# Kernel optimization log

Measured on AMD Instinct MI355X. Metric: run time of the kernel, lower is better.

The kernel has to match this reference:

```python
import jax, jax.numpy as jnp
import numpy as np

H, DK, DV, D = 16, 64, 64, 1024  # num_heads, dk, dv, model_dim (H*DV == D)
B, S = 4, 2048

def setup_inputs() -> dict:
    key = jax.random.key(0)
    ks = jax.random.split(key, 10)
    sc = 0.02
    x  = jax.random.normal(ks[0], (B, S, D), dtype=jnp.float32)
    Wq = jax.random.normal(ks[1], (H, D, DK), dtype=jnp.float32) * sc
    bq = jax.random.normal(ks[2], (H, DK), dtype=jnp.float32) * sc
    Wk = jax.random.normal(ks[3], (H, D, DK), dtype=jnp.float32) * sc
    bk = jax.random.normal(ks[4], (H, DK), dtype=jnp.float32) * sc
    Wv = jax.random.normal(ks[5], (H, D, DV), dtype=jnp.float32) * sc
    bv = jax.random.normal(ks[6], (H, DV), dtype=jnp.float32) * sc
    Wo = jax.random.normal(ks[7], (H * DV, D), dtype=jnp.float32) * sc
    bo = jax.random.normal(ks[8], (D,), dtype=jnp.float32) * sc
    return {"x": x, "Wq": Wq, "bq": bq, "Wk": Wk, "bk": bk,
            "Wv": Wv, "bv": bv, "Wo": Wo, "bo": bo}

def reference(x, Wq, bq, Wk, bk, Wv, bv, Wo, bo):
    # Batched per-head projections: [B,S,D] x [H,D,dk] -> [B,H,S,dk]
    Qx = jnp.einsum('bsd,hdk->bhsk', x, Wq) + bq[None, :, None, :]
    Kx = jnp.einsum('bsd,hdk->bhsk', x, Wk) + bk[None, :, None, :]
    Vx = jnp.einsum('bsd,hdv->bhsv', x, Wv) + bv[None, :, None, :]
    scores = jnp.einsum('bhsk,bhtk->bhst', Qx, Kx) / jnp.sqrt(jnp.float32(DK))
    attn = jax.nn.softmax(scores, axis=-1)
    out = jnp.einsum('bhst,bhtv->bhsv', attn, Vx)  # [B,H,S,dv]
    # concat heads (head order matches the torch cat order) -> [B,S,H*dv]
    cat = out.transpose(0, 2, 1, 3).reshape(B, S, H * DV)
    return cat @ Wo + bo
```

## Files before the change

kernel.cpp:

```cpp
#include <hip/hip_runtime.h>
#include <hip/hip_bf16.h>
#include <stdint.h>

typedef __bf16 bf16;
typedef __bf16 bf16x8 __attribute__((ext_vector_type(8)));
typedef __bf16 bf16x4 __attribute__((ext_vector_type(4)));
typedef float  f32x4  __attribute__((ext_vector_type(4)));
typedef float  f32x16 __attribute__((ext_vector_type(16)));

#define H_   16
#define D_   1024
#define B_   4
#define S_   2048
#define M_   (B_*S_)
#define REGION 8388608LL

#define QSCALE 0.18033688011112042f


__global__ void cast_x_kernel(const float* __restrict__ x, bf16* __restrict__ xb) {
    const int i = blockIdx.x * 256 + threadIdx.x;
    const float4* src = reinterpret_cast<const float4*>(x) + (size_t)i * 2;
    float4 a = src[0], b = src[1];
    bf16x8 o;
    o[0]=(bf16)a.x; o[1]=(bf16)a.y; o[2]=(bf16)a.z; o[3]=(bf16)a.w;
    o[4]=(bf16)b.x; o[5]=(bf16)b.y; o[6]=(bf16)b.z; o[7]=(bf16)b.w;
    *reinterpret_cast<bf16x8*>(xb + (size_t)i * 8) = o;
}

__global__ void prep_wqkv_kernel(const float* __restrict__ Wq, const float* __restrict__ Wk,
                                 const float* __restrict__ Wv, const float* __restrict__ bq,
                                 const float* __restrict__ bk, const float* __restrict__ bv,
                                 bf16* __restrict__ WqkvT, float* __restrict__ qkvb) {
    const int t = blockIdx.x * 256 + threadIdx.x;
    const int n = t >> 7, d0 = (t & 127) << 3;
    const int which = n >> 10, hh = (n >> 6) & 15, dk = n & 63;
    const float* W = (which == 0) ? Wq : (which == 1) ? Wk : Wv;
    const float* src = W + (size_t)hh * 65536 + (size_t)d0 * 64 + dk;
    bf16x8 o;
#pragma unroll
    for (int i = 0; i < 8; ++i) o[i] = (bf16)src[(size_t)i * 64];
    *reinterpret_cast<bf16x8*>(WqkvT + (size_t)n * D_ + d0) = o;
    if (d0 == 0) {
        const float* bb = (which == 0) ? bq : (which == 1) ? bk : bv;
        qkvb[n] = bb[n & 1023];
    }
}

__global__ void prep_wo_kernel(const float* __restrict__ Wo, bf16* __restrict__ WoT) {
    __shared__ float tile[64][65];
    const int k0 = blockIdx.x * 64, n0 = blockIdx.y * 64;
    const int t = threadIdx.x;
#pragma unroll
    for (int i = 0; i < 16; ++i) {
        int idx = t + i * 256, r = idx >> 6, c = idx & 63;
        tile[r][c] = Wo[(size_t)(k0 + r) * D_ + n0 + c];
    }
    __syncthreads();
#pragma unroll
    for (int i = 0; i < 16; ++i) {
        int idx = t + i * 256, n = idx >> 6, k = idx & 63;
        WoT[(size_t)(n0 + n) * D_ + k0 + k] = (bf16)tile[k][n];
    }
}

template <int MODE>
__global__ __launch_bounds__(256, 2)
void gemm_kernel(const bf16* __restrict__ A, const bf16* __restrict__ Bt,
                 const float* __restrict__ bias, void* __restrict__ Cout) {
    const int K = 1024;
    __shared__ __attribute__((aligned(16))) uint8_t ldsb[32768];
    const int t = threadIdx.x, w = t >> 6, ln = t & 63;
    const int g = ln >> 4, c = ln & 15;
    const int wm = w >> 1, wn = w & 1;
    const int bm = blockIdx.x, bn = blockIdx.y;

    const bf16* Ab = A  + (size_t)bm * 128 * K;
    const bf16* Bb = Bt + (size_t)bn * 128 * K;

    f32x4 zero = {0.f, 0.f, 0.f, 0.f};
    f32x4 acc[4][4];
#pragma unroll
    for (int mi = 0; mi < 4; ++mi)
#pragma unroll
        for (int ni = 0; ni < 4; ++ni) acc[mi][ni] = zero;

    const int srow = ln >> 3;
    const int scol = ((ln & 7) ^ srow) * 8;

    for (int kt = 0; kt < 16; ++kt) {
        const int k0 = kt * 64;
        __syncthreads();
#pragma unroll
        for (int i = 0; i < 4; ++i) {
            const int call = w * 4 + i;
            const int row = call * 8 + srow;
            const bf16* ga = Ab + (size_t)row * K + k0 + scol;
            const bf16* gb = Bb + (size_t)row * K + k0 + scol;
            __builtin_amdgcn_global_load_lds(
                (const __attribute__((address_space(1))) void*)ga,
                (__attribute__((address_space(3))) void*)(ldsb + call * 1024), 16, 0, 0);
            __builtin_amdgcn_global_load_lds(
                (const __attribute__((address_space(1))) void*)gb,
                (__attribute__((address_space(3))) void*)(ldsb + 16384 + call * 1024), 16, 0, 0);
        }
        __syncthreads();
#pragma unroll
        for (int kc = 0; kc < 2; ++kc) {
            bf16x8 af[4], bfr[4];
#pragma unroll
            for (int mi = 0; mi < 4; ++mi) {
                const int lrow = wm * 64 + mi * 16 + c;
                const int cb = (kc * 64 + g * 16) ^ ((lrow & 7) << 4);
                af[mi] = *reinterpret_cast<const bf16x8*>(ldsb + lrow * 128 + cb);
            }
#pragma unroll
            for (int ni = 0; ni < 4; ++ni) {
                const int lrow = wn * 64 + ni * 16 + c;
                const int cb = (kc * 64 + g * 16) ^ ((lrow & 7) << 4);
                bfr[ni] = *reinterpret_cast<const bf16x8*>(ldsb + 16384 + lrow * 128 + cb);
            }
#pragma unroll
            for (int mi = 0; mi < 4; ++mi)
#pragma unroll
                for (int ni = 0; ni < 4; ++ni)
                    acc[mi][ni] = __builtin_amdgcn_mfma_f32_16x16x32_bf16(
                        af[mi], bfr[ni], acc[mi][ni], 0, 0, 0);
        }
    }

#pragma unroll
    for (int mi = 0; mi < 4; ++mi) {
#pragma unroll
        for (int ni = 0; ni < 4; ++ni) {
            const int mrow = bm * 128 + wm * 64 + mi * 16 + g * 4;
            const int ncol = bn * 128 + wn * 64 + ni * 16 + c;
            const float bv_ = bias[ncol];
            if (MODE == 0) {
                const int which = ncol >> 10, hh = (ncol >> 6) & 15, dk = ncol & 63;
                const size_t bh64 = (size_t)((mrow >> 11) * 16 + hh);
                const int sI = mrow & 2047;
                if (which == 2) {
                    bf16x4 p4;
#pragma unroll
                    for (int j = 0; j < 4; ++j) p4[j] = (bf16)(acc[mi][ni][j] + bv_);
                    *reinterpret_cast<bf16x4*>((bf16*)Cout + 2 * REGION +
                                               (bh64 * 64 + dk) * S_ + sI) = p4;
                } else {
                    const float sc = (which == 0) ? QSCALE : 1.0f;
                    bf16* dst = (bf16*)Cout + (size_t)which * REGION +
                                (bh64 * S_ + sI) * 64 + dk;
#pragma unroll
                    for (int j = 0; j < 4; ++j)
                        dst[(size_t)j * 64] = (bf16)((acc[mi][ni][j] + bv_) * sc);
                }
            } else {
#pragma unroll
                for (int j = 0; j < 4; ++j)
                    ((float*)Cout)[(size_t)(mrow + j) * D_ + ncol] = acc[mi][ni][j] + bv_;
            }
        }
    }
}


__global__ __launch_bounds__(256, 4)
void attn_kernel(const bf16* __restrict__ Q, const bf16* __restrict__ K,
                 const bf16* __restrict__ Vt, bf16* __restrict__ cat) {
    __shared__ __attribute__((aligned(16))) bf16 KsA[2][64 * 64];
    __shared__ __attribute__((aligned(16))) bf16 VsA[2][64 * 64];
    __shared__ float red[4][32];
    const int t = threadIdx.x, w = t >> 6, lane = t & 63;
    const int l31 = lane & 31, h = lane >> 5;

    const int bid = blockIdx.x;
    const int nid = (bid & 7) * 128 + (bid >> 3);
    const int bh = nid >> 4, qb = nid & 15;
    const int q0 = qb * 128 + w * 32;

    const bf16* Qg = Q  + ((size_t)bh * S_ + q0) * 64;
    const bf16* Kg = K  + (size_t)bh * S_ * 64;
    const bf16* Vg = Vt + (size_t)bh * 64 * S_;

    bf16x8 qf[4];
#pragma unroll
    for (int dc = 0; dc < 4; ++dc)
        qf[dc] = *reinterpret_cast<const bf16x8*>(Qg + (size_t)l31 * 64 + dc * 16 + h * 8);

    const int sr = lane >> 3, ss = lane & 7;
    const int swz = (ss ^ sr) * 8;

    auto STAGE_KV = [&](int buf, int kv0) {
#pragma unroll
        for (int cc = 0; cc < 2; ++cc) {
            const int row = w * 16 + cc * 8;
            const int rr = row + sr;
            const int rs = (rr & ~12) | ((rr & 4) << 1) | ((rr & 8) >> 1);
            __builtin_amdgcn_global_load_lds(
                (const __attribute__((address_space(1))) void*)
                    (Kg + (size_t)(kv0 + rs) * 64 + swz),
                (__attribute__((address_space(3))) void*)(&KsA[buf][row * 64]), 16, 0, 0);
            __builtin_amdgcn_global_load_lds(
                (const __attribute__((address_space(1))) void*)
                    (Vg + (size_t)(rr) * S_ + kv0 + swz),
                (__attribute__((address_space(3))) void*)(&VsA[buf][row * 64]), 16, 0, 0);
        }
    };

    f32x16 o0, o1;
#pragma unroll
    for (int j = 0; j < 16; ++j) { o0[j] = 0.f; o1[j] = 0.f; }
    float lsum = 0.f;

    STAGE_KV(0, 0);
    for (int it = 0; it < 32; ++it) {
        __syncthreads();
        if (it + 1 < 32) STAGE_KV((it + 1) & 1, (it + 1) * 64);
        const bf16* ks = KsA[it & 1];
        const bf16* vs = VsA[it & 1];
#pragma unroll
        for (int kb = 0; kb < 2; ++kb) {
            f32x16 s;
#pragma unroll
            for (int j = 0; j < 16; ++j) s[j] = 0.f;
#pragma unroll
            for (int dc = 0; dc < 4; ++dc) {
                const int row = kb * 32 + l31;
                const int slot = (2 * dc + h) ^ (row & 7);
                bf16x8 kf = *reinterpret_cast<const bf16x8*>(ks + row * 64 + slot * 8);
                s = __builtin_amdgcn_mfma_f32_32x32x16_bf16(kf, qf[dc], s, 0, 0, 0);
            }
            float pf[16];
#pragma unroll
            for (int j = 0; j < 16; ++j) {
                pf[j] = __builtin_amdgcn_exp2f(s[j]);
                lsum += pf[j];
            }
            bf16x8 af0, af1;
#pragma unroll
            for (int e = 0; e < 8; ++e) { af0[e] = (bf16)pf[e]; af1[e] = (bf16)pf[8 + e]; }
#pragma unroll
            for (int t2 = 0; t2 < 2; ++t2) {
#pragma unroll
                for (int nb = 0; nb < 2; ++nb) {
                    const int row = l31 + 32 * nb;
                    const int slot = (4 * kb + 2 * t2 + h) ^ (row & 7);
                    bf16x8 vf = *reinterpret_cast<const bf16x8*>(vs + row * 64 + slot * 8);
                    if (nb == 0)
                        o0 = __builtin_amdgcn_mfma_f32_32x32x16_bf16(
                            t2 ? af1 : af0, vf, o0, 0, 0, 0);
                    else
                        o1 = __builtin_amdgcn_mfma_f32_32x32x16_bf16(
                            t2 ? af1 : af0, vf, o1, 0, 0, 0);
                }
            }
        }
    }

    lsum += __shfl_xor(lsum, 32, 64);
    if (h == 0) red[w][l31] = 1.0f / lsum;
    const int b = bh >> 4, hh = bh & 15;
#pragma unroll
    for (int j = 0; j < 16; ++j) {
        const int q = (j & 3) + 8 * (j >> 2) + 4 * h;
        const float rr = red[w][q];
        bf16* dst = cat + ((size_t)b * S_ + q0 + q) * D_ + hh * 64 + l31;
        dst[0]  = (bf16)(o0[j] * rr);
        dst[32] = (bf16)(o1[j] * rr);
    }
}

extern "C" void kernel_launch(void* const* d_in, const int* in_sizes, int n_in,
                              void* d_out, int out_size, void* d_ws, size_t ws_size,
                              hipStream_t stream) {
    const float* x  = (const float*)d_in[0];
    const float* Wq = (const float*)d_in[1];
    const float* bq = (const float*)d_in[2];
    const float* Wk = (const float*)d_in[3];
    const float* bk = (const float*)d_in[4];
    const float* Wv = (const float*)d_in[5];
    const float* bv = (const float*)d_in[6];
    const float* Wo = (const float*)d_in[7];
    const float* bo = (const float*)d_in[8];
    float* out = (float*)d_out;
    char* ws = (char*)d_ws;

    bf16*  xb    = (bf16*)(ws);
    bf16*  cat   = (bf16*)(ws + 16777216LL);
    bf16*  WqkvT = (bf16*)(ws + 33554432LL);
    bf16*  WoT   = (bf16*)(ws + 39845888LL);
    float* qkvb  = (float*)(ws + 41943040LL);
    bf16*  Qb    = (bf16*)(ws + 41955328LL);
    bf16*  Kb    = Qb + REGION;
    bf16*  Vtb   = Qb + 2 * REGION;

    hipLaunchKernelGGL(cast_x_kernel, dim3(4096), dim3(256), 0, stream, x, xb);
    hipLaunchKernelGGL(prep_wqkv_kernel, dim3(1536), dim3(256), 0, stream,
                       Wq, Wk, Wv, bq, bk, bv, WqkvT, qkvb);
    hipLaunchKernelGGL(prep_wo_kernel, dim3(16, 16), dim3(256), 0, stream, Wo, WoT);
    hipLaunchKernelGGL((gemm_kernel<0>), dim3(64, 24), dim3(256), 0, stream,
                       xb, WqkvT, qkvb, (void*)Qb);
    hipLaunchKernelGGL(attn_kernel, dim3(1024), dim3(256), 0, stream, Qb, Kb, Vtb, cat);
    hipLaunchKernelGGL((gemm_kernel<1>), dim3(64, 8), dim3(256), 0, stream,
                       cat, WoT, bo, (void*)out);
}
```

Baseline: 191.2 us.

## Process two query tiles per wave in attention to reuse K/V fragments

Each wave in the attention kernel now handles 64 query rows as two 32-row MFMA tiles instead of one. K and V fragments read from LDS are shared across both tiles, roughly halving LDS traffic per unit of MFMA work. The grid halves to 512 blocks, launch bounds drop to 2 blocks per CU, and s_setprio hints are wrapped around the MFMA bursts. The cost is more accumulator registers per thread and fewer blocks to hide latency.

After: 192.2 us. About the same (+0.5%).

```diff
diff --git a/kernel.cpp b/kernel.cpp
--- a/kernel.cpp
+++ b/kernel.cpp
@@ -164,28 +164,31 @@
 }
 
 
-__global__ __launch_bounds__(256, 4)
+__global__ __launch_bounds__(256, 2)
 void attn_kernel(const bf16* __restrict__ Q, const bf16* __restrict__ K,
                  const bf16* __restrict__ Vt, bf16* __restrict__ cat) {
     __shared__ __attribute__((aligned(16))) bf16 KsA[2][64 * 64];
     __shared__ __attribute__((aligned(16))) bf16 VsA[2][64 * 64];
-    __shared__ float red[4][32];
+    __shared__ float red[4][64];
     const int t = threadIdx.x, w = t >> 6, lane = t & 63;
     const int l31 = lane & 31, h = lane >> 5;
 
     const int bid = blockIdx.x;
-    const int nid = (bid & 7) * 128 + (bid >> 3);
-    const int bh = nid >> 4, qb = nid & 15;
-    const int q0 = qb * 128 + w * 32;
+    const int nid = (bid & 7) * 64 + (bid >> 3);
+    const int bh = nid >> 3, qb = nid & 7;
+    const int q0 = qb * 256 + w * 64;
 
     const bf16* Qg = Q  + ((size_t)bh * S_ + q0) * 64;
     const bf16* Kg = K  + (size_t)bh * S_ * 64;
     const bf16* Vg = Vt + (size_t)bh * 64 * S_;
 
-    bf16x8 qf[4];
-#pragma unroll
-    for (int dc = 0; dc < 4; ++dc)
-        qf[dc] = *reinterpret_cast<const bf16x8*>(Qg + (size_t)l31 * 64 + dc * 16 + h * 8);
+    bf16x8 qf[2][4];
+#pragma unroll
+    for (int qt = 0; qt < 2; ++qt)
+#pragma unroll
+        for (int dc = 0; dc < 4; ++dc)
+            qf[qt][dc] = *reinterpret_cast<const bf16x8*>(
+                Qg + (size_t)(qt * 32 + l31) * 64 + dc * 16 + h * 8);
 
     const int sr = lane >> 3, ss = lane & 7;
     const int swz = (ss ^ sr) * 8;
@@ -207,10 +210,13 @@
         }
     };
 
-    f32x16 o0, o1;
-#pragma unroll
-    for (int j = 0; j < 16; ++j) { o0[j] = 0.f; o1[j] = 0.f; }
-    float lsum = 0.f;
+    f32x16 o[2][2];
+    f32x16 lsv[2];
+#pragma unroll
+    for (int qt = 0; qt < 2; ++qt) {
+#pragma unroll
+        for (int j = 0; j < 16; ++j) { o[qt][0][j] = 0.f; o[qt][1][j] = 0.f; lsv[qt][j] = 0.f; }
+    }
 
     STAGE_KV(0, 0);
     for (int it = 0; it < 32; ++it) {
@@ -220,25 +226,37 @@
         const bf16* vs = VsA[it & 1];
 #pragma unroll
         for (int kb = 0; kb < 2; ++kb) {
-            f32x16 s;
-#pragma unroll
-            for (int j = 0; j < 16; ++j) s[j] = 0.f;
+            bf16x8 kf[4];
 #pragma unroll
             for (int dc = 0; dc < 4; ++dc) {
                 const int row = kb * 32 + l31;
                 const int slot = (2 * dc + h) ^ (row & 7);
-                bf16x8 kf = *reinterpret_cast<const bf16x8*>(ks + row * 64 + slot * 8);
-                s = __builtin_amdgcn_mfma_f32_32x32x16_bf16(kf, qf[dc], s, 0, 0, 0);
-            }
-            float pf[16];
-#pragma unroll
-            for (int j = 0; j < 16; ++j) {
-                pf[j] = __builtin_amdgcn_exp2f(s[j]);
-                lsum += pf[j];
-            }
-            bf16x8 af0, af1;
-#pragma unroll
-            for (int e = 0; e < 8; ++e) { af0[e] = (bf16)pf[e]; af1[e] = (bf16)pf[8 + e]; }
+                kf[dc] = *reinterpret_cast<const bf16x8*>(ks + row * 64 + slot * 8);
+            }
+            f32x16 s0, s1;
+#pragma unroll
+            for (int j = 0; j < 16; ++j) { s0[j] = 0.f; s1[j] = 0.f; }
+            __builtin_amdgcn_s_setprio(1);
+#pragma unroll
+            for (int dc = 0; dc < 4; ++dc) {
+                s0 = __builtin_amdgcn_mfma_f32_32x32x16_bf16(kf[dc], qf[0][dc], s0, 0, 0, 0);
+                s1 = __builtin_amdgcn_mfma_f32_32x32x16_bf16(kf[dc], qf[1][dc], s1, 0, 0, 0);
+            }
+            __builtin_amdgcn_s_setprio(0);
+            f32x16 p0, p1;
+#pragma unroll
+            for (int j = 0; j < 16; ++j) p0[j] = __builtin_amdgcn_exp2f(s0[j]);
+#pragma unroll
+            for (int j = 0; j < 16; ++j) p1[j] = __builtin_amdgcn_exp2f(s1[j]);
+            lsv[0] += p0;
+            lsv[1] += p1;
+            bf16x8 a00, a01, a10, a11;
+#pragma unroll
+            for (int e = 0; e < 8; ++e) {
+                a00[e] = (bf16)p0[e]; a01[e] = (bf16)p0[8 + e];
+                a10[e] = (bf16)p1[e]; a11[e] = (bf16)p1[8 + e];
+            }
+            __builtin_amdgcn_s_setprio(1);
 #pragma unroll
             for (int t2 = 0; t2 < 2; ++t2) {
 #pragma unroll
@@ -246,28 +264,35 @@
                     const int row = l31 + 32 * nb;
                     const int slot = (4 * kb + 2 * t2 + h) ^ (row & 7);
                     bf16x8 vf = *reinterpret_cast<const bf16x8*>(vs + row * 64 + slot * 8);
-                    if (nb == 0)
-                        o0 = __builtin_amdgcn_mfma_f32_32x32x16_bf16(
-                            t2 ? af1 : af0, vf, o0, 0, 0, 0);
-                    else
-                        o1 = __builtin_amdgcn_mfma_f32_32x32x16_bf16(
-                            t2 ? af1 : af0, vf, o1, 0, 0, 0);
+                    o[0][nb] = __builtin_amdgcn_mfma_f32_32x32x16_bf16(
+                        t2 ? a01 : a00, vf, o[0][nb], 0, 0, 0);
+                    o[1][nb] = __builtin_amdgcn_mfma_f32_32x32x16_bf16(
+                        t2 ? a11 : a10, vf, o[1][nb], 0, 0, 0);
                 }
             }
-        }
-    }
-
-    lsum += __shfl_xor(lsum, 32, 64);
-    if (h == 0) red[w][l31] = 1.0f / lsum;
+            __builtin_amdgcn_s_setprio(0);
+        }
+    }
+
+#pragma unroll
+    for (int qt = 0; qt < 2; ++qt) {
+        float s = 0.f;
+#pragma unroll
+        for (int j = 0; j < 16; ++j) s += lsv[qt][j];
+        s += __shfl_xor(s, 32, 64);
+        if (h == 0) red[w][qt * 32 + l31] = 1.0f / s;
+    }
     const int b = bh >> 4, hh = bh & 15;
 #pragma unroll
-    for (int j = 0; j < 16; ++j) {
-        const int q = (j & 3) + 8 * (j >> 2) + 4 * h;
-        const float rr = red[w][q];
-        bf16* dst = cat + ((size_t)b * S_ + q0 + q) * D_ + hh * 64 + l31;
-        dst[0]  = (bf16)(o0[j] * rr);
-        dst[32] = (bf16)(o1[j] * rr);
-    }
+    for (int qt = 0; qt < 2; ++qt)
+#pragma unroll
+        for (int j = 0; j < 16; ++j) {
+            const int q = qt * 32 + (j & 3) + 8 * (j >> 2) + 4 * h;
+            const float rr = red[w][q];
+            bf16* dst = cat + ((size_t)b * S_ + q0 + q) * D_ + hh * 64 + l31;
+            dst[0]  = (bf16)(o[qt][0][j] * rr);
+            dst[32] = (bf16)(o[qt][1][j] * rr);
+        }
 }
 
 extern "C" void kernel_launch(void* const* d_in, const int* in_sizes, int n_in,
@@ -300,7 +325,7 @@
     hipLaunchKernelGGL(prep_wo_kernel, dim3(16, 16), dim3(256), 0, stream, Wo, WoT);
     hipLaunchKernelGGL((gemm_kernel<0>), dim3(64, 24), dim3(256), 0, stream,
                        xb, WqkvT, qkvb, (void*)Qb);
-    hipLaunchKernelGGL(attn_kernel, dim3(1024), dim3(256), 0, stream, Qb, Kb, Vtb, cat);
+    hipLaunchKernelGGL(attn_kernel, dim3(512), dim3(256), 0, stream, Qb, Kb, Vtb, cat);
     hipLaunchKernelGGL((gemm_kernel<1>), dim3(64, 8), dim3(256), 0, stream,
                        cat, WoT, bo, (void*)out);
 }
```
